# Kernel tuning notes

Hardware: AMD Instinct MI355X
Metric: run time of the kernel (lower is better)

## Reference

```python
import jax, jax.numpy as jnp
import numpy as np

N = 65536      # num ref nodes
M = 65536      # num query nodes
E = 1572864    # num edges (avg degree 24)
K0 = 27        # num kernels (3x3x3 neighborhood)
D1 = 64        # input channels
D2 = 64        # output channels


def setup_inputs() -> dict:
    key = jax.random.key(0)
    k1, k2, k3, k4, k5, k6 = jax.random.split(key, 6)
    # kernel init mirrors initialize_kernel_weight (uniform in [-bound, bound])
    fan_in = D1 * K0
    gain = float(np.sqrt(2.0 / (1.0 + 5.0)))  # leaky_relu gain with slope sqrt(5)
    std = gain / np.sqrt(fan_in)
    bound = float(np.sqrt(3.0) * std)
    kernel = jax.random.uniform(k1, (K0, D1, D2), minval=-bound, maxval=bound, dtype=jnp.float32)
    ref_feat = jax.random.normal(k2, (N, D1), dtype=jnp.float32)
    e_kernel = jax.random.randint(k3, (E,), 0, K0)
    e_ref = jax.random.randint(k4, (E,), 0, N)
    e_query = jax.random.randint(k5, (E,), 0, M)
    e_weight = jax.random.uniform(k6, (E,), dtype=jnp.float32)
    return {
        "kernel": kernel,
        "ref_feat": ref_feat,
        "e_kernel": e_kernel,
        "e_ref": e_ref,
        "e_query": e_query,
        "num_queries": M,
        "e_weight": e_weight,
    }


def reference(kernel, ref_feat, e_kernel, e_ref, e_query, num_queries, e_weight):
    # Math of MessagePassing.forward:
    #   query_feat[m] = sum_{edges e: e_query[e]==m} w_e * (ref_feat[e_ref[e]] @ kernel[e_kernel[e]])
    # Efficient form: precompute each node's transform under every kernel
    # (N*K0*D1*D2 dense GEMM), then gather per edge and scatter-reduce.
    transformed = jnp.einsum('nd,kdo->nko', ref_feat, kernel)   # [N, K0, D2]
    msgs = transformed[e_ref, e_kernel] * e_weight[:, None]      # [E, D2]
    query_feat = jax.ops.segment_sum(msgs, e_query, num_segments=num_queries)  # [M, D2]
    return query_feat
```

## Files before the change

kernel.cpp:

```cpp
#include <hip/hip_runtime.h>

#define DIN 64
#define DOUT 64
#define MAXK 32

typedef __bf16 bf16x8 __attribute__((ext_vector_type(8)));
typedef float  f32x4  __attribute__((ext_vector_type(4)));
typedef unsigned int u32x4 __attribute__((ext_vector_type(4)));

static __device__ inline unsigned short f2b(float x) {
    return __builtin_bit_cast(unsigned short, (__bf16)x);
}
static __device__ inline float b2f(unsigned short u) {
    return __uint_as_float(((unsigned int)u) << 16);
}


__global__ void conv_w_kernel(const float* __restrict__ W,
                              unsigned short* __restrict__ Wt, int total,
                              int* __restrict__ qcount) {
    int i = blockIdx.x * blockDim.x + threadIdx.x;
    if (i < 256) qcount[i] = 0;
    if (i < total) {
        int j    = i & 7;
        int lane = (i >> 3) & 63;
        int h    = (i >> 9) & 1;
        int t    = (i >> 10) & 3;
        int k    = i >> 12;
        int col  = lane & 15;
        int quad = lane >> 4;
        int d1 = h * 32 + quad * 8 + j;
        int d2 = t * 16 + col;
        Wt[i] = f2b(W[(k * 64 + d1) * 64 + d2]);
    }
}


#define KSPLIT 4

__global__ __launch_bounds__(256) void phaseA_v3_kernel(
    const float* __restrict__ ref,
    const unsigned short* __restrict__ Wt,
    unsigned short* __restrict__ T,
    int K0, int Nn)
{
    const int lane = threadIdx.x & 63;
    const int wid  = threadIdx.x >> 6;
    const int col  = lane & 15;
    const int quad = lane >> 4;
    const int n0   = blockIdx.x * 64 + wid * 16;
    const int row  = n0 + col;

    const int kch = (K0 + KSPLIT - 1) / KSPLIT;
    const int k0  = blockIdx.y * kch;
    int k1 = k0 + kch;
    if (k1 > K0) k1 = K0;

    __shared__ __align__(16) char ldsbuf[4 * 2 * 2304];
    char* bufs = ldsbuf + wid * 2 * 2304;

    const float* rp = ref + (size_t)row * 64;
    f32x4 r0 = *reinterpret_cast<const f32x4*>(rp + quad * 8);
    f32x4 r1 = *reinterpret_cast<const f32x4*>(rp + quad * 8 + 4);
    f32x4 r2 = *reinterpret_cast<const f32x4*>(rp + 32 + quad * 8);
    f32x4 r3 = *reinterpret_cast<const f32x4*>(rp + 32 + quad * 8 + 4);
    bf16x8 b0, b1;
    #pragma unroll
    for (int i = 0; i < 4; ++i) {
        b0[i]     = (__bf16)r0[i];
        b0[4 + i] = (__bf16)r1[i];
        b1[i]     = (__bf16)r2[i];
        b1[4 + i] = (__bf16)r3[i];
    }

    const int rrow = lane >> 2;
    const int rq   = lane & 3;

    for (int k = k0; k < k1; ++k) {
        char* buf = bufs + (k & 1) * 2304;
        const unsigned short* Wk = Wt + (size_t)k * 4096;
        #pragma unroll
        for (int t = 0; t < 4; ++t) {
            const unsigned short* ap = Wk + (size_t)t * 1024 + lane * 8;
            bf16x8 a0 = *reinterpret_cast<const bf16x8*>(ap);
            bf16x8 a1 = *reinterpret_cast<const bf16x8*>(ap + 512);
            f32x4 c = {0.f, 0.f, 0.f, 0.f};
            c = __builtin_amdgcn_mfma_f32_16x16x32_bf16(a0, b0, c, 0, 0, 0);
            c = __builtin_amdgcn_mfma_f32_16x16x32_bf16(a1, b1, c, 0, 0, 0);
            unsigned int lo = (unsigned int)f2b(c[0]) | ((unsigned int)f2b(c[1]) << 16);
            unsigned int hi = (unsigned int)f2b(c[2]) | ((unsigned int)f2b(c[3]) << 16);
            *reinterpret_cast<uint2*>(buf + col * 144 + t * 32 + quad * 8) =
                make_uint2(lo, hi);
        }
        u32x4 v0 = *reinterpret_cast<const u32x4*>(buf + rrow * 144 + rq * 32);
        u32x4 v1 = *reinterpret_cast<const u32x4*>(buf + rrow * 144 + rq * 32 + 16);
        size_t gbase = ((size_t)k * Nn + n0 + rrow) * 64 + rq * 16;
        *reinterpret_cast<u32x4*>(T + gbase)     = v0;
        *reinterpret_cast<u32x4*>(T + gbase + 8) = v1;
    }
}


__global__ void p1_hist_kernel(const int* __restrict__ eq, int E,
                               int* __restrict__ qcount) {
    __shared__ int l[256];
    l[threadIdx.x] = 0;
    __syncthreads();
    int stride = gridDim.x * blockDim.x;
    for (int i = blockIdx.x * blockDim.x + threadIdx.x; i < E; i += stride)
        atomicAdd(&l[((unsigned)eq[i]) >> 8], 1);
    __syncthreads();
    int v = l[threadIdx.x];
    if (v) atomicAdd(&qcount[threadIdx.x], v);
}

__global__ void p1_scan_kernel(const int* __restrict__ qcount,
                               int* __restrict__ gbase, int* __restrict__ gcursor,
                               int* __restrict__ qstart, int NB, int M, int E) {
    __shared__ int sh[256];
    int t = threadIdx.x;
    int v = (t < NB) ? qcount[t] : 0;
    sh[t] = v;
    __syncthreads();
    #pragma unroll
    for (int o = 1; o < 256; o <<= 1) {
        int x = (t >= o) ? sh[t - o] : 0;
        __syncthreads();
        sh[t] += x;
        __syncthreads();
    }
    int ex = sh[t] - v;
    if (t < NB) { gbase[t] = ex; gcursor[t] = ex; }
    if (t == 0) qstart[M] = E;
}

__global__ __launch_bounds__(256) void p1_scatter_kernel(
    const int* __restrict__ eq, const int* __restrict__ er,
    const int* __restrict__ ek, const float* __restrict__ ew,
    int E, int* __restrict__ gcursor, uint2* __restrict__ tmp)
{
    __shared__ int bin[256];
    __shared__ int base[256];
    const int t = threadIdx.x;
    bin[t] = 0;
    __syncthreads();
    const int i0 = blockIdx.x * 4096;
    unsigned key[16];
    unsigned rank[16];
    uint2 pay[16];
    #pragma unroll
    for (int u = 0; u < 16; ++u) {
        int i = i0 + u * 256 + t;
        if (i < E) {
            int q = eq[i];
            unsigned b = ((unsigned)q) >> 8;
            key[u] = b;
            rank[u] = atomicAdd(&bin[b], 1);
            pay[u] = make_uint2((unsigned)er[i] | ((unsigned)ek[i] << 16) |
                                ((unsigned)(q & 255) << 21),
                                __float_as_uint(ew[i]));
        } else {
            key[u] = 0xFFFFFFFFu;
        }
    }
    __syncthreads();
    int c = bin[t];
    if (c) base[t] = atomicAdd(&gcursor[t], c);
    __syncthreads();
    #pragma unroll
    for (int u = 0; u < 16; ++u) {
        if (key[u] != 0xFFFFFFFFu)
            tmp[(size_t)base[key[u]] + rank[u]] = pay[u];
    }
}

__global__ __launch_bounds__(256) void p2_kernel(
    const uint2* __restrict__ tmp, const int* __restrict__ gbase,
    const int* __restrict__ qcount, uint2* __restrict__ rec,
    int* __restrict__ qstart)
{
    __shared__ int fine[256];
    __shared__ int foff[256];
    const int b = blockIdx.x;
    const int t = threadIdx.x;
    const int s = gbase[b];
    const int L = qcount[b];
    fine[t] = 0;
    __syncthreads();
    for (int i = t; i < L; i += 256)
        atomicAdd(&fine[(tmp[s + i].x >> 21) & 255], 1);
    __syncthreads();
    int v = fine[t];
    __syncthreads();
    #pragma unroll
    for (int o = 1; o < 256; o <<= 1) {
        int x = (t >= o) ? fine[t - o] : 0;
        __syncthreads();
        fine[t] += x;
        __syncthreads();
    }
    foff[t] = fine[t] - v;
    qstart[b * 256 + t] = s + foff[t];
    __syncthreads();
    fine[t] = 0;
    __syncthreads();
    for (int i = t; i < L; i += 256) {
        uint2 p = tmp[s + i];
        unsigned fb = (p.x >> 21) & 255;
        int r = atomicAdd(&fine[fb], 1);
        rec[(size_t)s + foff[fb] + r] = p;
    }
}


__global__ __launch_bounds__(256) void phaseB_kernel(
    const unsigned short* __restrict__ T,
    const uint2* __restrict__ rec,
    const int* __restrict__ qstart,
    float* __restrict__ out, int Nn)
{
    const int lane = threadIdx.x & 63;
    const int wid  = threadIdx.x >> 6;
    const int q    = blockIdx.x * 4 + wid;

    int beg = qstart[q];
    int end = qstart[q + 1];
    int cnt = end - beg;
    float acc = 0.f;

    if (cnt <= 64) {
        uint2 rv = make_uint2(0u, 0u);
        if (lane < cnt) rv = rec[beg + lane];
        int j = 0;
        for (; j + 8 <= cnt; j += 8) {
            float partial[8];
            #pragma unroll
            for (int u = 0; u < 8; ++u) {
                unsigned mx = (unsigned)__builtin_amdgcn_readlane((int)rv.x, j + u);
                unsigned mw = (unsigned)__builtin_amdgcn_readlane((int)rv.y, j + u);
                unsigned off = (((mx >> 16) & 31) * (unsigned)Nn + (mx & 0xFFFFu)) * 64u
                               + (unsigned)lane;
                partial[u] = __uint_as_float(mw) * b2f(T[off]);
            }
            #pragma unroll
            for (int u = 0; u < 8; ++u) acc += partial[u];
        }
        for (; j < cnt; ++j) {
            unsigned mx = (unsigned)__builtin_amdgcn_readlane((int)rv.x, j);
            unsigned mw = (unsigned)__builtin_amdgcn_readlane((int)rv.y, j);
            unsigned off = (((mx >> 16) & 31) * (unsigned)Nn + (mx & 0xFFFFu)) * 64u
                           + (unsigned)lane;
            acc = fmaf(__uint_as_float(mw), b2f(T[off]), acc);
        }
    } else {
        for (int j = beg; j < end; ++j) {
            uint2 v0 = rec[j];
            unsigned m0 = __builtin_amdgcn_readfirstlane(v0.x);
            float w0 = __uint_as_float(__builtin_amdgcn_readfirstlane(v0.y));
            unsigned off = (((m0 >> 16) & 31) * (unsigned)Nn + (m0 & 0xFFFFu)) * 64u
                           + (unsigned)lane;
            acc = fmaf(w0, b2f(T[off]), acc);
        }
    }
    out[(size_t)q * 64 + lane] = acc;
}


__global__ void hist_kernel(const int* __restrict__ ek, int E, int* __restrict__ counts) {
    __shared__ int l[MAXK];
    if (threadIdx.x < MAXK) l[threadIdx.x] = 0;
    __syncthreads();
    int stride = gridDim.x * blockDim.x;
    for (int i = blockIdx.x * blockDim.x + threadIdx.x; i < E; i += stride)
        atomicAdd(&l[ek[i]], 1);
    __syncthreads();
    if (threadIdx.x < MAXK) {
        int v = l[threadIdx.x];
        if (v) atomicAdd(&counts[threadIdx.x], v);
    }
}

__global__ void scan_kernel(const int* __restrict__ counts, int K,
                            int* __restrict__ start, int* __restrict__ cursor) {
    if (threadIdx.x == 0 && blockIdx.x == 0) {
        int acc = 0;
        for (int k = 0; k < K; ++k) {
            start[k] = acc;
            cursor[k] = acc;
            acc += counts[k];
        }
    }
}

__global__ void scatter_kernel(const int* __restrict__ ek, int E,
                               int* __restrict__ cursor, int* __restrict__ sorted) {
    __shared__ int lcnt[MAXK], lbase[MAXK], lpos[MAXK];
    if (threadIdx.x < MAXK) { lcnt[threadIdx.x] = 0; lpos[threadIdx.x] = 0; }
    __syncthreads();
    int i = blockIdx.x * blockDim.x + threadIdx.x;
    int k = 0;
    bool valid = (i < E);
    if (valid) { k = ek[i]; atomicAdd(&lcnt[k], 1); }
    __syncthreads();
    if (threadIdx.x < MAXK) {
        int v = lcnt[threadIdx.x];
        if (v) lbase[threadIdx.x] = atomicAdd(&cursor[threadIdx.x], v);
    }
    __syncthreads();
    if (valid) {
        int slot = lbase[k] + atomicAdd(&lpos[k], 1);
        sorted[slot] = i;
    }
}

__global__ __launch_bounds__(256) void mp_bucket_kernel(
    const float* __restrict__ W, const float* __restrict__ ref,
    const int* __restrict__ e_ref, const int* __restrict__ e_query,
    const float* __restrict__ e_weight, const int* __restrict__ sorted,
    const int* __restrict__ start, const int* __restrict__ counts,
    float* __restrict__ out)
{
    const int k = blockIdx.y;
    const int lane = threadIdx.x & 63;
    const int wid = threadIdx.x >> 6;

    float wreg[DIN];
    const float* Wk = W + k * DIN * DOUT;
    #pragma unroll
    for (int d = 0; d < DIN; ++d) wreg[d] = Wk[d * DOUT + lane];

    const int s = start[k];
    const int c = counts[k];
    const int nwaves = gridDim.x * 4;

    for (int i = blockIdx.x * 4 + wid; i < c; i += nwaves) {
        int eid = __builtin_amdgcn_readfirstlane(sorted[s + i]);
        int r = e_ref[eid];
        int q = e_query[eid];
        float w = e_weight[eid];
        const float* row = ref + r * DIN;
        float a0 = 0.f, a1 = 0.f, a2 = 0.f, a3 = 0.f;
        #pragma unroll
        for (int d = 0; d < DIN; d += 4) {
            a0 += row[d + 0] * wreg[d + 0];
            a1 += row[d + 1] * wreg[d + 1];
            a2 += row[d + 2] * wreg[d + 2];
            a3 += row[d + 3] * wreg[d + 3];
        }
        atomicAdd(&out[q * DOUT + lane], ((a0 + a1) + (a2 + a3)) * w);
    }
}


extern "C" void kernel_launch(void* const* d_in, const int* in_sizes, int n_in,
                              void* d_out, int out_size, void* d_ws, size_t ws_size,
                              hipStream_t stream) {
    const float* W        = (const float*)d_in[0];
    const float* ref      = (const float*)d_in[1];
    const int*   e_kernel = (const int*)d_in[2];
    const int*   e_ref    = (const int*)d_in[3];
    const int*   e_query  = (const int*)d_in[4];
    const float* e_weight = (const float*)d_in[6];

    const int K0 = in_sizes[0] / (DIN * DOUT);
    const int N  = in_sizes[1] / DIN;
    const int E  = in_sizes[2];
    const int M  = out_size / DOUT;
    const int KD = K0 * 64;
    const int NB = M / 256;

    float* out = (float*)d_out;

    size_t off = 0;
    auto alloc = [&](size_t bytes, size_t align) {
        off = (off + align - 1) / align * align;
        size_t r = off; off += bytes; return r;
    };
    size_t o_tmp     = alloc((size_t)E * 8, 16);
    size_t o_rec     = alloc((size_t)E * 8, 16);
    size_t o_qstart  = alloc((size_t)(M + 1) * 4, 4);
    size_t o_qcount  = alloc(256 * 4, 4);
    size_t o_gbase   = alloc(256 * 4, 4);
    size_t o_gcursor = alloc(256 * 4, 4);
    size_t o_wt      = alloc((size_t)K0 * 4096 * 2, 16);
    size_t o_T       = alloc((size_t)N * KD * 2, 16);
    size_t needA = off;

    bool planA_ok = (ws_size >= needA) && (M % 256 == 0) && (NB >= 1) && (NB <= 256) &&
                    (N % 64 == 0) && (N <= 65536) && (K0 <= 32);

    if (planA_ok) {
        char* ws = (char*)d_ws;
        uint2* tmp           = (uint2*)(ws + o_tmp);
        uint2* rec           = (uint2*)(ws + o_rec);
        int*  qstart         = (int*)(ws + o_qstart);
        int*  qcount         = (int*)(ws + o_qcount);
        int*  gbase          = (int*)(ws + o_gbase);
        int*  gcursor        = (int*)(ws + o_gcursor);
        unsigned short* Wt   = (unsigned short*)(ws + o_wt);
        unsigned short* T    = (unsigned short*)(ws + o_T);

        conv_w_kernel<<<(K0 * 4096 + 255) / 256, 256, 0, stream>>>(W, Wt, K0 * 4096,
                                                                   qcount);
        p1_hist_kernel<<<512, 256, 0, stream>>>(e_query, E, qcount);
        p1_scan_kernel<<<1, 256, 0, stream>>>(qcount, gbase, gcursor, qstart, NB, M, E);
        p1_scatter_kernel<<<(E + 4095) / 4096, 256, 0, stream>>>(e_query, e_ref, e_kernel,
                                                                 e_weight, E, gcursor, tmp);
        p2_kernel<<<NB, 256, 0, stream>>>(tmp, gbase, qcount, rec, qstart);

        dim3 agrid(N / 64, KSPLIT);
        phaseA_v3_kernel<<<agrid, 256, 0, stream>>>(ref, Wt, T, K0, N);

        phaseB_kernel<<<M / 4, 256, 0, stream>>>(T, rec, qstart, out, N);
    } else {
        hipMemsetAsync(out, 0, (size_t)out_size * sizeof(float), stream);
        size_t needB = (size_t)(96 + E) * sizeof(int);
        if (ws_size >= needB) {
            int* ws_i   = (int*)d_ws;
            int* counts = ws_i;
            int* start  = ws_i + 32;
            int* cursor = ws_i + 64;
            int* sorted = ws_i + 96;
            hipMemsetAsync(counts, 0, 96 * sizeof(int), stream);
            hist_kernel<<<512, 256, 0, stream>>>(e_kernel, E, counts);
            scan_kernel<<<1, 64, 0, stream>>>(counts, K0, start, cursor);
            scatter_kernel<<<(E + 255) / 256, 256, 0, stream>>>(e_kernel, E, cursor, sorted);
            dim3 grid(64, K0);
            mp_bucket_kernel<<<grid, 256, 0, stream>>>(W, ref, e_ref, e_query, e_weight,
                                                       sorted, start, counts, out);
        }
    }
}
```

Measured before the change: 283.3 us.

## Use finer 64-query buckets for two-level edge sort and split phaseA wider

```diff
diff --git a/kernel.cpp b/kernel.cpp
--- a/kernel.cpp
+++ b/kernel.cpp
@@ -18,9 +18,9 @@
 
 __global__ void conv_w_kernel(const float* __restrict__ W,
                               unsigned short* __restrict__ Wt, int total,
-                              int* __restrict__ qcount) {
+                              int* __restrict__ qcount, int NB) {
     int i = blockIdx.x * blockDim.x + threadIdx.x;
-    if (i < 256) qcount[i] = 0;
+    if (i < NB) qcount[i] = 0;
     if (i < total) {
         int j    = i & 7;
         int lane = (i >> 3) & 63;
@@ -36,7 +36,7 @@
 }
 
 
-#define KSPLIT 4
+#define KSPLIT 8
 
 __global__ __launch_bounds__(256) void phaseA_v3_kernel(
     const float* __restrict__ ref,
@@ -103,27 +103,32 @@
 
 __global__ void p1_hist_kernel(const int* __restrict__ eq, int E,
                                int* __restrict__ qcount) {
-    __shared__ int l[256];
-    l[threadIdx.x] = 0;
+    __shared__ int l[1024];
+    const int t = threadIdx.x;
+    #pragma unroll
+    for (int s4 = 0; s4 < 4; ++s4) l[t + s4 * 256] = 0;
     __syncthreads();
     int stride = gridDim.x * blockDim.x;
-    for (int i = blockIdx.x * blockDim.x + threadIdx.x; i < E; i += stride)
-        atomicAdd(&l[((unsigned)eq[i]) >> 8], 1);
-    __syncthreads();
-    int v = l[threadIdx.x];
-    if (v) atomicAdd(&qcount[threadIdx.x], v);
+    for (int i = blockIdx.x * blockDim.x + t; i < E; i += stride)
+        atomicAdd(&l[((unsigned)eq[i]) >> 6], 1);
+    __syncthreads();
+    #pragma unroll
+    for (int s4 = 0; s4 < 4; ++s4) {
+        int v = l[t + s4 * 256];
+        if (v) atomicAdd(&qcount[t + s4 * 256], v);
+    }
 }
 
 __global__ void p1_scan_kernel(const int* __restrict__ qcount,
                                int* __restrict__ gbase, int* __restrict__ gcursor,
                                int* __restrict__ qstart, int NB, int M, int E) {
-    __shared__ int sh[256];
+    __shared__ int sh[1024];
     int t = threadIdx.x;
     int v = (t < NB) ? qcount[t] : 0;
     sh[t] = v;
     __syncthreads();
     #pragma unroll
-    for (int o = 1; o < 256; o <<= 1) {
+    for (int o = 1; o < 1024; o <<= 1) {
         int x = (t >= o) ? sh[t - o] : 0;
         __syncthreads();
         sh[t] += x;
@@ -139,10 +144,11 @@
     const int* __restrict__ ek, const float* __restrict__ ew,
     int E, int* __restrict__ gcursor, uint2* __restrict__ tmp)
 {
-    __shared__ int bin[256];
-    __shared__ int base[256];
+    __shared__ int bin[1024];
+    __shared__ int base[1024];
     const int t = threadIdx.x;
-    bin[t] = 0;
+    #pragma unroll
+    for (int s4 = 0; s4 < 4; ++s4) bin[t + s4 * 256] = 0;
     __syncthreads();
     const int i0 = blockIdx.x * 4096;
     unsigned key[16];
@@ -153,19 +159,23 @@
         int i = i0 + u * 256 + t;
         if (i < E) {
             int q = eq[i];
-            unsigned b = ((unsigned)q) >> 8;
+            unsigned b = ((unsigned)q) >> 6;
             key[u] = b;
             rank[u] = atomicAdd(&bin[b], 1);
             pay[u] = make_uint2((unsigned)er[i] | ((unsigned)ek[i] << 16) |
-                                ((unsigned)(q & 255) << 21),
+                                ((unsigned)(q & 63) << 21),
                                 __float_as_uint(ew[i]));
         } else {
             key[u] = 0xFFFFFFFFu;
         }
     }
     __syncthreads();
-    int c = bin[t];
-    if (c) base[t] = atomicAdd(&gcursor[t], c);
+    #pragma unroll
+    for (int s4 = 0; s4 < 4; ++s4) {
+        int bb = t + s4 * 256;
+        int c = bin[bb];
+        if (c) base[bb] = atomicAdd(&gcursor[bb], c);
+    }
     __syncthreads();
     #pragma unroll
     for (int u = 0; u < 16; ++u) {
@@ -179,34 +189,33 @@
     const int* __restrict__ qcount, uint2* __restrict__ rec,
     int* __restrict__ qstart)
 {
-    __shared__ int fine[256];
-    __shared__ int foff[256];
+    __shared__ int fine[64];
+    __shared__ int foff[64];
     const int b = blockIdx.x;
     const int t = threadIdx.x;
     const int s = gbase[b];
     const int L = qcount[b];
-    fine[t] = 0;
+    if (t < 64) fine[t] = 0;
     __syncthreads();
     for (int i = t; i < L; i += 256)
-        atomicAdd(&fine[(tmp[s + i].x >> 21) & 255], 1);
-    __syncthreads();
-    int v = fine[t];
-    __syncthreads();
-    #pragma unroll
-    for (int o = 1; o < 256; o <<= 1) {
-        int x = (t >= o) ? fine[t - o] : 0;
-        __syncthreads();
-        fine[t] += x;
-        __syncthreads();
-    }
-    foff[t] = fine[t] - v;
-    qstart[b * 256 + t] = s + foff[t];
-    __syncthreads();
-    fine[t] = 0;
+        atomicAdd(&fine[(tmp[s + i].x >> 21) & 63], 1);
+    __syncthreads();
+    if (t < 64) {
+        int v = fine[t];
+        int x = v;
+        #pragma unroll
+        for (int o = 1; o < 64; o <<= 1) {
+            int y = __shfl_up(x, o);
+            if (t >= o) x += y;
+        }
+        foff[t] = x - v;
+        qstart[b * 64 + t] = s + x - v;
+        fine[t] = 0;
+    }
     __syncthreads();
     for (int i = t; i < L; i += 256) {
         uint2 p = tmp[s + i];
-        unsigned fb = (p.x >> 21) & 255;
+        unsigned fb = (p.x >> 21) & 63;
         int r = atomicAdd(&fine[fb], 1);
         rec[(size_t)s + foff[fb] + r] = p;
     }
@@ -367,7 +376,7 @@
     const int E  = in_sizes[2];
     const int M  = out_size / DOUT;
     const int KD = K0 * 64;
-    const int NB = M / 256;
+    const int NB = M / 64;
 
     float* out = (float*)d_out;
 
@@ -379,14 +388,14 @@
     size_t o_tmp     = alloc((size_t)E * 8, 16);
     size_t o_rec     = alloc((size_t)E * 8, 16);
     size_t o_qstart  = alloc((size_t)(M + 1) * 4, 4);
-    size_t o_qcount  = alloc(256 * 4, 4);
-    size_t o_gbase   = alloc(256 * 4, 4);
-    size_t o_gcursor = alloc(256 * 4, 4);
+    size_t o_qcount  = alloc(1024 * 4, 4);
+    size_t o_gbase   = alloc(1024 * 4, 4);
+    size_t o_gcursor = alloc(1024 * 4, 4);
     size_t o_wt      = alloc((size_t)K0 * 4096 * 2, 16);
     size_t o_T       = alloc((size_t)N * KD * 2, 16);
     size_t needA = off;
 
-    bool planA_ok = (ws_size >= needA) && (M % 256 == 0) && (NB >= 1) && (NB <= 256) &&
+    bool planA_ok = (ws_size >= needA) && (M % 64 == 0) && (NB >= 1) && (NB <= 1024) &&
                     (N % 64 == 0) && (N <= 65536) && (K0 <= 32);
 
     if (planA_ok) {
@@ -400,10 +409,11 @@
         unsigned short* Wt   = (unsigned short*)(ws + o_wt);
         unsigned short* T    = (unsigned short*)(ws + o_T);
 
-        conv_w_kernel<<<(K0 * 4096 + 255) / 256, 256, 0, stream>>>(W, Wt, K0 * 4096,
-                                                                   qcount);
+        int zgrid = (K0 * 4096 > NB) ? K0 * 4096 : NB;
+        conv_w_kernel<<<(zgrid + 255) / 256, 256, 0, stream>>>(W, Wt, K0 * 4096,
+                                                               qcount, NB);
         p1_hist_kernel<<<512, 256, 0, stream>>>(e_query, E, qcount);
-        p1_scan_kernel<<<1, 256, 0, stream>>>(qcount, gbase, gcursor, qstart, NB, M, E);
+        p1_scan_kernel<<<1, 1024, 0, stream>>>(qcount, gbase, gcursor, qstart, NB, M, E);
         p1_scatter_kernel<<<(E + 4095) / 4096, 256, 0, stream>>>(e_query, e_ref, e_kernel,
                                                                  e_weight, E, gcursor, tmp);
         p2_kernel<<<NB, 256, 0, stream>>>(tmp, gbase, qcount, rec, qstart);
```

New measurement: 287.5 us. About the same (+1.5%).
